# Kernel tuning notes

Measured on AMD Instinct MI355X. Metric: run time of the kernel, lower is better.

Reference implementation:

```python
import jax, jax.numpy as jnp
import numpy as np

B, T, C = 16, 64, 512


def setup_inputs() -> dict:
    key = jax.random.key(0)
    ks = jax.random.split(key, 12)
    s = 1.0 / np.sqrt(C)
    st = 1.0 / np.sqrt(2.0)
    return {
        "x": jax.random.normal(ks[0], (B, T, C), dtype=jnp.float32),
        "ts": jax.random.uniform(ks[1], (B, T), dtype=jnp.float32),
        "attn_mask": jnp.ones((B, T), dtype=jnp.float32),
        # project: Linear(C, C)
        "W_proj": jax.random.uniform(ks[2], (C, C), jnp.float32, -s, s),
        "b_proj": jax.random.uniform(ks[3], (C,), jnp.float32, -s, s),
        # embed_xs: Linear(C, C)
        "W_x": jax.random.uniform(ks[4], (C, C), jnp.float32, -s, s),
        "b_x": jax.random.uniform(ks[5], (C,), jnp.float32, -s, s),
        # embed_ts: Linear(2, C)
        "W_t": jax.random.uniform(ks[6], (2, C), jnp.float32, -st, st),
        "b_t": jax.random.uniform(ks[7], (C,), jnp.float32, -st, st),
        # get_importances Linear(C, C)
        "W_imp": jax.random.uniform(ks[8], (C, C), jnp.float32, -s, s),
        "b_imp": jax.random.uniform(ks[9], (C,), jnp.float32, -s, s),
    }


def reference(x, ts, attn_mask, W_proj, b_proj, W_x, b_x, W_t, b_t, W_imp, b_imp):
    # x: [B,T,C], ts: [B,T], attn_mask: [B,T]
    values = (x @ W_proj + b_proj)[:, None, :, :]          # [B,1,T,C]
    rel = ts[:, :, None] - ts[:, None, :]                  # [B,T,T]
    rel2 = jnp.log1p(jnp.maximum(jnp.stack([rel, -rel], axis=-1), 0.0))  # [B,T,T,2]
    h = rel2 @ W_t + b_t                                   # [B,T,T,C] (include_t)
    h = h + (x @ W_x + b_x)[:, None, :, :]                 # include_x, broadcast over dim 1
    importances = jax.nn.sigmoid(jax.nn.relu(h) @ W_imp + b_imp)  # [B,T,T,C]
    importances = importances * attn_mask[:, None, :, None]
    interactions = jax.nn.logsumexp(values * importances, axis=2)  # [B,T,C]
    return (x + interactions, importances.mean(axis=3))
```

## Files before the change

### kernel.cpp

```cpp
#include <hip/hip_runtime.h>
#include <hip/hip_bf16.h>

#define Bn 16
#define Tn 64
#define Cn 512
#define LDA  520
#define LDA8 528

#define LOG2E 1.4426950408889634f
#define LN2   0.6931471805599453f
#define ASC 16.0f
#define WSC 256.0f
#define ZSC (1.0f/4096.0f)
#define NZL (-(LOG2E)*(ZSC))
#define SC1 0x7F7F7F7FU

typedef short s8v __attribute__((ext_vector_type(8)));
typedef float f4v __attribute__((ext_vector_type(4)));
typedef int   i8v __attribute__((ext_vector_type(8)));

__device__ __forceinline__ unsigned int pk2bf(float a, float b){
  __hip_bfloat162 t = __float22bfloat162_rn(make_float2(a, b));
  union { __hip_bfloat162 h; unsigned int u; } c; c.h = t; return c.u;
}
__device__ __forceinline__ float bits2f(unsigned int u){
  union { unsigned int u; float f; } c; c.u = u; return c.f;
}
__device__ __forceinline__ s8v pack_bf8(const float* v){
  union { uint4 u; s8v s; } c;
  c.u.x = pk2bf(v[0], v[1]); c.u.y = pk2bf(v[2], v[3]);
  c.u.z = pk2bf(v[4], v[5]); c.u.w = pk2bf(v[6], v[7]);
  return c.s;
}
union U8 { uint4 q[2]; i8v v; };

__global__ __launch_bounds__(512)
void pre(const float* __restrict__ x, const float* __restrict__ ts,
         const float* __restrict__ Wp, const float* __restrict__ bp,
         const float* __restrict__ Wx, const float* __restrict__ bx,
         const float* __restrict__ bt, const float* __restrict__ Wi,
         float* __restrict__ xe, unsigned short* __restrict__ vfrag,
         unsigned char* __restrict__ Wsw8, float* __restrict__ R){
  __shared__ unsigned short lA[Tn * LDA];
  const int blk = blockIdx.x;
  const int tid = threadIdx.x;
  if(blk < 32){
    int gid2 = blk * 512 + tid;
    float r[8];
#pragma unroll
    for(int q = 0; q < 4; ++q){
      int p = gid2 * 4 + q;
      int b = p >> 12, i = (p >> 6) & 63, j = p & 63;
      float d = ts[b * Tn + i] - ts[b * Tn + j];
      r[2*q]   = __logf(1.f + fmaxf(d, 0.f));
      r[2*q+1] = __logf(1.f + fmaxf(-d, 0.f));
    }
    float4* Rf4 = reinterpret_cast<float4*>(R);
    Rf4[gid2 * 2    ] = make_float4(r[0], r[1], r[2], r[3]);
    Rf4[gid2 * 2 + 1] = make_float4(r[4], r[5], r[6], r[7]);
    return;
  }
  if(blk < 64){
    int rem = (blk - 32) * 512 + tid;
    int p    = rem & 1;
    int lane = (rem >> 1) & 63;
    int t    = (rem >> 7) & 31;
    int s128 = rem >> 12;
    int quad = lane >> 4, ln = lane & 15;
    int k0 = s128 * 128 + quad * 32 + p * 16;
    int n  = t * 16 + ln;
    float v[16];
#pragma unroll
    for(int j = 0; j < 16; ++j) v[j] = Wi[(k0 + j) * Cn + n] * WSC;
    unsigned int d[4];
#pragma unroll
    for(int g = 0; g < 4; ++g){
      int dd = __builtin_amdgcn_cvt_pk_fp8_f32(v[4*g],   v[4*g+1], 0, false);
      dd     = __builtin_amdgcn_cvt_pk_fp8_f32(v[4*g+2], v[4*g+3], dd, true);
      d[g] = (unsigned int)dd;
    }
    uint4 o; o.x = d[0]; o.y = d[1]; o.z = d[2]; o.w = d[3];
    *reinterpret_cast<uint4*>(Wsw8 + (size_t)(s128 * 32 + t) * 2048 + p * 1024 + lane * 16) = o;
    return;
  }
  const int idx = blk - 64;
  const int b = idx >> 3, mat = (idx >> 2) & 1, half = idx & 3;
  const int lane = tid & 63, w = tid >> 6, quad = lane >> 4, ln = lane & 15;
  const int t = half * 8 + w;
  const float* Wg = mat ? Wx : Wp;
  const float* wb = Wg + (size_t)(quad * 8) * Cn + t * 16 + ln;

  const int c0 = (tid & 127) * 4, jb = tid >> 7;
#pragma unroll
  for(int it = 0; it < 16; ++it){
    int j = jb + it * 4;
    f4v xv = *reinterpret_cast<const f4v*>(x + ((b * Tn + j) * Cn + c0));
    uint2 uu; uu.x = pk2bf(xv[0], xv[1]); uu.y = pk2bf(xv[2], xv[3]);
    *reinterpret_cast<uint2*>(&lA[j * LDA + c0]) = uu;
  }
  float wv[8];
#pragma unroll
  for(int j = 0; j < 8; ++j) wv[j] = wb[j * Cn];
  __syncthreads();

  s8v a[4], an[4];
#pragma unroll
  for(int mt = 0; mt < 4; ++mt)
    a[mt] = *reinterpret_cast<const s8v*>(&lA[(mt * 16 + ln) * LDA + quad * 8]);
  f4v acc[4];
#pragma unroll
  for(int mt = 0; mt < 4; ++mt){ acc[mt][0]=0.f; acc[mt][1]=0.f; acc[mt][2]=0.f; acc[mt][3]=0.f; }
  s8v bcur = pack_bf8(wv);

#pragma unroll 2
  for(int s = 0; s < 16; ++s){
    int sn = (s + 1) & 15;
    float wn[8];
#pragma unroll
    for(int j = 0; j < 8; ++j) wn[j] = wb[(size_t)sn * 32 * Cn + j * Cn];
#pragma unroll
    for(int mt = 0; mt < 4; ++mt)
      an[mt] = *reinterpret_cast<const s8v*>(&lA[(mt * 16 + ln) * LDA + sn * 32 + quad * 8]);
#pragma unroll
    for(int mt = 0; mt < 4; ++mt)
      acc[mt] = __builtin_amdgcn_mfma_f32_16x16x32_bf16(a[mt], bcur, acc[mt], 0, 0, 0);
#pragma unroll
    for(int mt = 0; mt < 4; ++mt) a[mt] = an[mt];
    bcur = pack_bf8(wn);
  }

  const int c = t * 16 + ln;
  const int oct = t >> 2, w2 = t & 3;
  if(mat == 0){
    float bb = bp[c];
    const int eb_h = w2 & 1;
#pragma unroll
    for(int mt = 0; mt < 4; ++mt){
      float v0 = (acc[mt][0] + bb) * LOG2E;
      float v1 = (acc[mt][1] + bb) * LOG2E;
      float v2 = (acc[mt][2] + bb) * LOG2E;
      float v3 = (acc[mt][3] + bb) * LOG2E;
      uint2 o; o.x = pk2bf(v0, v1); o.y = pk2bf(v2, v3);
      int eb = mt * 2 + (w2 >> 1);
      *reinterpret_cast<uint2*>(vfrag + ((size_t)((b * 8 + oct) * 8 + eb) * 64 + lane) * 8 + eb_h * 4) = o;
    }
  } else {
    float bb = bx[c] + bt[c];
#pragma unroll
    for(int mt = 0; mt < 4; ++mt)
#pragma unroll
      for(int r = 0; r < 4; ++r){
        int j = mt * 16 + quad * 4 + r;
        xe[(b * Tn + j) * Cn + c] = (acc[mt][r] + bb) * ASC;
      }
  }
}

__global__ __launch_bounds__(512, 4)
void fused(const float* __restrict__ x, const float* __restrict__ am,
           const float* __restrict__ Wt, const float* __restrict__ bimp,
           const unsigned char* __restrict__ Wsw8, const float* __restrict__ R,
           const float* __restrict__ xe, const unsigned short* __restrict__ vfrag,
           float* __restrict__ out0, float* __restrict__ out1){
  __shared__ unsigned char lA8[Tn * LDA8];
  __shared__ float msk[Tn], rr0[Tn], rr1[Tn], rsum[Tn];
  const int b = blockIdx.x >> 6, i = blockIdx.x & 63;
  const int tid = threadIdx.x;
  const int lane = tid & 63, w = tid >> 6, quad = lane >> 4, ln = lane & 15;
  const int st = blockIdx.x & 3;

  float mv = 0.f; float2 rv = make_float2(0.f, 0.f);
  if(tid < Tn){
    mv = am[b * Tn + tid];
    rv = reinterpret_cast<const float2*>(R)[(b * Tn + i) * Tn + tid];
  }

  const int c0 = (tid & 127) * 4, jb = tid >> 7;
  f4v xv[16];
#pragma unroll
  for(int it = 0; it < 16; ++it)
    xv[it] = *reinterpret_cast<const f4v*>(xe + ((b * Tn + (jb + it * 4)) * Cn + c0));

  if(tid < Tn){ msk[tid] = mv; rr0[tid] = rv.x; rr1[tid] = rv.y; rsum[tid] = 0.f; }
  __syncthreads();

  f4v wt0 = *reinterpret_cast<const f4v*>(Wt + c0);
  f4v wt1 = *reinterpret_cast<const f4v*>(Wt + Cn + c0);
  wt0[0]*=ASC; wt0[1]*=ASC; wt0[2]*=ASC; wt0[3]*=ASC;
  wt1[0]*=ASC; wt1[1]*=ASC; wt1[2]*=ASC; wt1[3]*=ASC;
#pragma unroll
  for(int it = 0; it < 16; ++it){
    int j = jb + it * 4;
    float r0 = rr0[j], r1 = rr1[j];
    float h0 = fmaxf(fmaf(r1, wt1[0], fmaf(r0, wt0[0], xv[it][0])), 0.f);
    float h1 = fmaxf(fmaf(r1, wt1[1], fmaf(r0, wt0[1], xv[it][1])), 0.f);
    float h2 = fmaxf(fmaf(r1, wt1[2], fmaf(r0, wt0[2], xv[it][2])), 0.f);
    float h3 = fmaxf(fmaf(r1, wt1[3], fmaf(r0, wt0[3], xv[it][3])), 0.f);
    int d = __builtin_amdgcn_cvt_pk_fp8_f32(h0, h1, 0, false);
    d     = __builtin_amdgcn_cvt_pk_fp8_f32(h2, h3, d, true);
    *reinterpret_cast<int*>(lA8 + j * LDA8 + c0) = d;
  }
  __syncthreads();

  f4v acc[4][4];
#pragma unroll
  for(int mt = 0; mt < 4; ++mt)
#pragma unroll
    for(int nt = 0; nt < 4; ++nt){
      acc[mt][nt][0]=0.f; acc[mt][nt][1]=0.f; acc[mt][nt][2]=0.f; acc[mt][nt][3]=0.f;
    }

#pragma unroll 1
  for(int sI = 0; sI < 4; ++sI){
    const int s128 = (st + sI) & 3;
    U8 ub0, ub1, ub2, ub3;
    const unsigned char* Bb = Wsw8 + (size_t)(s128 * 32 + w * 4) * 2048 + lane * 16;
    ub0.q[0] = *reinterpret_cast<const uint4*>(Bb);
    ub0.q[1] = *reinterpret_cast<const uint4*>(Bb + 1024);
    ub1.q[0] = *reinterpret_cast<const uint4*>(Bb + 2048);
    ub1.q[1] = *reinterpret_cast<const uint4*>(Bb + 3072);
    ub2.q[0] = *reinterpret_cast<const uint4*>(Bb + 4096);
    ub2.q[1] = *reinterpret_cast<const uint4*>(Bb + 5120);
    ub3.q[0] = *reinterpret_cast<const uint4*>(Bb + 6144);
    ub3.q[1] = *reinterpret_cast<const uint4*>(Bb + 7168);
#pragma unroll
    for(int mt = 0; mt < 4; ++mt){
      U8 ua;
      const unsigned char* ap = lA8 + (mt * 16 + ln) * LDA8 + s128 * 128 + quad * 32;
      ua.q[0] = *reinterpret_cast<const uint4*>(ap);
      ua.q[1] = *reinterpret_cast<const uint4*>(ap + 16);
      acc[mt][0] = __builtin_amdgcn_mfma_scale_f32_16x16x128_f8f6f4(ua.v, ub0.v, acc[mt][0], 0, 0, 0, SC1, 0, SC1);
      acc[mt][1] = __builtin_amdgcn_mfma_scale_f32_16x16x128_f8f6f4(ua.v, ub1.v, acc[mt][1], 0, 0, 0, SC1, 0, SC1);
      acc[mt][2] = __builtin_amdgcn_mfma_scale_f32_16x16x128_f8f6f4(ua.v, ub2.v, acc[mt][2], 0, 0, 0, SC1, 0, SC1);
      acc[mt][3] = __builtin_amdgcn_mfma_scale_f32_16x16x128_f8f6f4(ua.v, ub3.v, acc[mt][3], 0, 0, 0, SC1, 0, SC1);
    }
  }

  uint4 vv[8];
#pragma unroll
  for(int eb = 0; eb < 8; ++eb)
    vv[eb] = *reinterpret_cast<const uint4*>(vfrag + ((size_t)((b * 8 + w) * 8 + eb) * 64 + lane) * 8);
  float xq[4];
#pragma unroll
  for(int nt = 0; nt < 4; ++nt)
    xq[nt] = x[(b * Tn + i) * Cn + (w * 64 + nt * 16 + ln)];

  const unsigned int* vw = reinterpret_cast<const unsigned int*>(vv);
  float bbf[4];
#pragma unroll
  for(int nt = 0; nt < 4; ++nt) bbf[nt] = bimp[w * 64 + nt * 16 + ln] * -LOG2E;
  float se[4] = {0.f, 0.f, 0.f, 0.f};
#pragma unroll
  for(int mt = 0; mt < 4; ++mt)
#pragma unroll
    for(int r = 0; r < 4; ++r){
      float mk = msk[mt * 16 + quad * 4 + r];
      float p = 0.f;
#pragma unroll
      for(int nt = 0; nt < 4; ++nt){
        float zn = fmaf(acc[mt][nt][r], NZL, bbf[nt]);
        float im = mk * __builtin_amdgcn_rcpf(1.f + __builtin_amdgcn_exp2f(zn));
        p += im;
        int e = mt * 16 + nt * 4 + r;
        unsigned int d = vw[e >> 1];
        float vl = bits2f((e & 1) ? (d & 0xffff0000u) : (d << 16));
        se[nt] += __builtin_amdgcn_exp2f(vl * im);
      }
      p += __shfl_xor(p, 1, 64);
      p += __shfl_xor(p, 2, 64);
      p += __shfl_xor(p, 4, 64);
      p += __shfl_xor(p, 8, 64);
      if(ln == 0) atomicAdd(&rsum[mt * 16 + quad * 4 + r], p);
    }
  __syncthreads();
  if(tid < Tn) out1[(b * Tn + i) * Tn + tid] = rsum[tid] * (1.f / 512.f);

#pragma unroll
  for(int nt = 0; nt < 4; ++nt){
    float s0 = se[nt];
    s0 += __shfl_xor(s0, 16, 64);
    s0 += __shfl_xor(s0, 32, 64);
    if(quad == 0){
      int idx = (b * Tn + i) * Cn + (w * 64 + nt * 16 + ln);
      out0[idx] = xq[nt] + __builtin_amdgcn_logf(s0) * LN2;
    }
  }
}

extern "C" void kernel_launch(void* const* d_in, const int* in_sizes, int n_in,
                              void* d_out, int out_size, void* d_ws, size_t ws_size,
                              hipStream_t stream){
  const float* x    = (const float*)d_in[0];
  const float* ts   = (const float*)d_in[1];
  const float* am   = (const float*)d_in[2];
  const float* Wp   = (const float*)d_in[3];
  const float* bp   = (const float*)d_in[4];
  const float* Wx   = (const float*)d_in[5];
  const float* bx   = (const float*)d_in[6];
  const float* Wt   = (const float*)d_in[7];
  const float* bt   = (const float*)d_in[8];
  const float* Wi   = (const float*)d_in[9];
  const float* bimp = (const float*)d_in[10];
  float* out0 = (float*)d_out;
  float* out1 = out0 + Bn * Tn * Cn;

  char* ws = (char*)d_ws;
  unsigned char*  Wsw8  = (unsigned char*)ws;
  float*          xe    = (float*)(ws + 262144);
  unsigned short* vfrag = (unsigned short*)(ws + 2359296);
  float*          R     = (float*)(ws + 3407872);

  pre<<<192, 512, 0, stream>>>(x, ts, Wp, bp, Wx, bx, bt, Wi, xe, vfrag, Wsw8, R);
  fused<<<1024, 512, 0, stream>>>(x, am, Wt, bimp, Wsw8, R, xe, vfrag, out0, out1);
}
```

Baseline: 118.9 us.

## Use 1024-thread blocks with 16 waves each owning 32 output columns and prefetch B

Doubles the block size of the fused kernel to 16 waves, so each wave computes a 64x32 tile instead of 64x64. This halves per-thread accumulators, B fragments and epilogue work. It also software-prefetches the next K-slice of the fp8 weight fragments into registers while the current MFMAs run. The goal is more latency hiding and lower register pressure per wave. The cost is heavier block-level synchronisation, and launch_bounds(1024,4) may force register spilling or cap occupancy.

```diff
diff --git a/kernel.cpp b/kernel.cpp
--- a/kernel.cpp
+++ b/kernel.cpp
@@ -156,7 +156,7 @@
   }
 }
 
-__global__ __launch_bounds__(512, 4)
+__global__ __launch_bounds__(1024, 4)
 void fused(const float* __restrict__ x, const float* __restrict__ am,
            const float* __restrict__ Wt, const float* __restrict__ bimp,
            const unsigned char* __restrict__ Wsw8, const float* __restrict__ R,
@@ -168,18 +168,28 @@
   const int tid = threadIdx.x;
   const int lane = tid & 63, w = tid >> 6, quad = lane >> 4, ln = lane & 15;
   const int st = blockIdx.x & 3;
+  const int bi = b * Tn + i;
 
   float mv = 0.f; float2 rv = make_float2(0.f, 0.f);
   if(tid < Tn){
     mv = am[b * Tn + tid];
-    rv = reinterpret_cast<const float2*>(R)[(b * Tn + i) * Tn + tid];
+    rv = reinterpret_cast<const float2*>(R)[(size_t)bi * Tn + tid];
+  }
+
+  U8 cb0, cb1;
+  {
+    const unsigned char* Bb = Wsw8 + (size_t)(st * 32 + w * 2) * 2048 + (size_t)lane * 16;
+    cb0.q[0] = *reinterpret_cast<const uint4*>(Bb);
+    cb0.q[1] = *reinterpret_cast<const uint4*>(Bb + 1024);
+    cb1.q[0] = *reinterpret_cast<const uint4*>(Bb + 2048);
+    cb1.q[1] = *reinterpret_cast<const uint4*>(Bb + 3072);
   }
 
   const int c0 = (tid & 127) * 4, jb = tid >> 7;
-  f4v xv[16];
-#pragma unroll
-  for(int it = 0; it < 16; ++it)
-    xv[it] = *reinterpret_cast<const f4v*>(xe + ((b * Tn + (jb + it * 4)) * Cn + c0));
+  f4v xv[8];
+#pragma unroll
+  for(int it = 0; it < 8; ++it)
+    xv[it] = *reinterpret_cast<const f4v*>(xe + ((size_t)(b * Tn + (jb + it * 8)) * Cn + c0));
 
   if(tid < Tn){ msk[tid] = mv; rr0[tid] = rv.x; rr1[tid] = rv.y; rsum[tid] = 0.f; }
   __syncthreads();
@@ -189,8 +199,8 @@
   wt0[0]*=ASC; wt0[1]*=ASC; wt0[2]*=ASC; wt0[3]*=ASC;
   wt1[0]*=ASC; wt1[1]*=ASC; wt1[2]*=ASC; wt1[3]*=ASC;
 #pragma unroll
-  for(int it = 0; it < 16; ++it){
-    int j = jb + it * 4;
+  for(int it = 0; it < 8; ++it){
+    int j = jb + it * 8;
     float r0 = rr0[j], r1 = rr1[j];
     float h0 = fmaxf(fmaf(r1, wt1[0], fmaf(r0, wt0[0], xv[it][0])), 0.f);
     float h1 = fmaxf(fmaf(r1, wt1[1], fmaf(r0, wt0[1], xv[it][1])), 0.f);
@@ -202,54 +212,53 @@
   }
   __syncthreads();
 
-  f4v acc[4][4];
+  f4v acc[4][2];
 #pragma unroll
   for(int mt = 0; mt < 4; ++mt)
 #pragma unroll
-    for(int nt = 0; nt < 4; ++nt){
+    for(int nt = 0; nt < 2; ++nt){
       acc[mt][nt][0]=0.f; acc[mt][nt][1]=0.f; acc[mt][nt][2]=0.f; acc[mt][nt][3]=0.f;
     }
 
 #pragma unroll 1
   for(int sI = 0; sI < 4; ++sI){
     const int s128 = (st + sI) & 3;
-    U8 ub0, ub1, ub2, ub3;
-    const unsigned char* Bb = Wsw8 + (size_t)(s128 * 32 + w * 4) * 2048 + lane * 16;
-    ub0.q[0] = *reinterpret_cast<const uint4*>(Bb);
-    ub0.q[1] = *reinterpret_cast<const uint4*>(Bb + 1024);
-    ub1.q[0] = *reinterpret_cast<const uint4*>(Bb + 2048);
-    ub1.q[1] = *reinterpret_cast<const uint4*>(Bb + 3072);
-    ub2.q[0] = *reinterpret_cast<const uint4*>(Bb + 4096);
-    ub2.q[1] = *reinterpret_cast<const uint4*>(Bb + 5120);
-    ub3.q[0] = *reinterpret_cast<const uint4*>(Bb + 6144);
-    ub3.q[1] = *reinterpret_cast<const uint4*>(Bb + 7168);
+    U8 nb0, nb1;
+    if(sI < 3){
+      const int sn = (st + sI + 1) & 3;
+      const unsigned char* Bn2 = Wsw8 + (size_t)(sn * 32 + w * 2) * 2048 + (size_t)lane * 16;
+      nb0.q[0] = *reinterpret_cast<const uint4*>(Bn2);
+      nb0.q[1] = *reinterpret_cast<const uint4*>(Bn2 + 1024);
+      nb1.q[0] = *reinterpret_cast<const uint4*>(Bn2 + 2048);
+      nb1.q[1] = *reinterpret_cast<const uint4*>(Bn2 + 3072);
+    }
 #pragma unroll
     for(int mt = 0; mt < 4; ++mt){
       U8 ua;
       const unsigned char* ap = lA8 + (mt * 16 + ln) * LDA8 + s128 * 128 + quad * 32;
       ua.q[0] = *reinterpret_cast<const uint4*>(ap);
       ua.q[1] = *reinterpret_cast<const uint4*>(ap + 16);
-      acc[mt][0] = __builtin_amdgcn_mfma_scale_f32_16x16x128_f8f6f4(ua.v, ub0.v, acc[mt][0], 0, 0, 0, SC1, 0, SC1);
-      acc[mt][1] = __builtin_amdgcn_mfma_scale_f32_16x16x128_f8f6f4(ua.v, ub1.v, acc[mt][1], 0, 0, 0, SC1, 0, SC1);
-      acc[mt][2] = __builtin_amdgcn_mfma_scale_f32_16x16x128_f8f6f4(ua.v, ub2.v, acc[mt][2], 0, 0, 0, SC1, 0, SC1);
-      acc[mt][3] = __builtin_amdgcn_mfma_scale_f32_16x16x128_f8f6f4(ua.v, ub3.v, acc[mt][3], 0, 0, 0, SC1, 0, SC1);
-    }
-  }
-
-  uint4 vv[8];
-#pragma unroll
-  for(int eb = 0; eb < 8; ++eb)
-    vv[eb] = *reinterpret_cast<const uint4*>(vfrag + ((size_t)((b * 8 + w) * 8 + eb) * 64 + lane) * 8);
-  float xq[4];
-#pragma unroll
-  for(int nt = 0; nt < 4; ++nt)
-    xq[nt] = x[(b * Tn + i) * Cn + (w * 64 + nt * 16 + ln)];
+      acc[mt][0] = __builtin_amdgcn_mfma_scale_f32_16x16x128_f8f6f4(ua.v, cb0.v, acc[mt][0], 0, 0, 0, SC1, 0, SC1);
+      acc[mt][1] = __builtin_amdgcn_mfma_scale_f32_16x16x128_f8f6f4(ua.v, cb1.v, acc[mt][1], 0, 0, 0, SC1, 0, SC1);
+    }
+    if(sI < 3){ cb0 = nb0; cb1 = nb1; }
+  }
+
+  uint4 vv[4];
+#pragma unroll
+  for(int mt = 0; mt < 4; ++mt)
+    vv[mt] = *reinterpret_cast<const uint4*>(
+        vfrag + ((size_t)((b * 8 + (w >> 1)) * 8 + (mt * 2 + (w & 1))) * 64 + lane) * 8);
+  float xq[2];
+#pragma unroll
+  for(int nt = 0; nt < 2; ++nt)
+    xq[nt] = x[(size_t)bi * Cn + (w * 32 + nt * 16 + ln)];
 
   const unsigned int* vw = reinterpret_cast<const unsigned int*>(vv);
-  float bbf[4];
-#pragma unroll
-  for(int nt = 0; nt < 4; ++nt) bbf[nt] = bimp[w * 64 + nt * 16 + ln] * -LOG2E;
-  float se[4] = {0.f, 0.f, 0.f, 0.f};
+  float bbf[2];
+#pragma unroll
+  for(int nt = 0; nt < 2; ++nt) bbf[nt] = bimp[w * 32 + nt * 16 + ln] * -LOG2E;
+  float se[2] = {0.f, 0.f};
 #pragma unroll
   for(int mt = 0; mt < 4; ++mt)
 #pragma unroll
@@ -257,13 +266,12 @@
       float mk = msk[mt * 16 + quad * 4 + r];
       float p = 0.f;
 #pragma unroll
-      for(int nt = 0; nt < 4; ++nt){
+      for(int nt = 0; nt < 2; ++nt){
         float zn = fmaf(acc[mt][nt][r], NZL, bbf[nt]);
         float im = mk * __builtin_amdgcn_rcpf(1.f + __builtin_amdgcn_exp2f(zn));
         p += im;
-        int e = mt * 16 + nt * 4 + r;
-        unsigned int d = vw[e >> 1];
-        float vl = bits2f((e & 1) ? (d & 0xffff0000u) : (d << 16));
+        unsigned int d = vw[mt * 4 + nt * 2 + (r >> 1)];
+        float vl = bits2f((r & 1) ? (d & 0xffff0000u) : (d << 16));
         se[nt] += __builtin_amdgcn_exp2f(vl * im);
       }
       p += __shfl_xor(p, 1, 64);
@@ -273,15 +281,15 @@
       if(ln == 0) atomicAdd(&rsum[mt * 16 + quad * 4 + r], p);
     }
   __syncthreads();
-  if(tid < Tn) out1[(b * Tn + i) * Tn + tid] = rsum[tid] * (1.f / 512.f);
-
-#pragma unroll
-  for(int nt = 0; nt < 4; ++nt){
+  if(tid < Tn) out1[(size_t)bi * Tn + tid] = rsum[tid] * (1.f / 512.f);
+
+#pragma unroll
+  for(int nt = 0; nt < 2; ++nt){
     float s0 = se[nt];
     s0 += __shfl_xor(s0, 16, 64);
     s0 += __shfl_xor(s0, 32, 64);
     if(quad == 0){
-      int idx = (b * Tn + i) * Cn + (w * 64 + nt * 16 + ln);
+      int idx = bi * Cn + (w * 32 + nt * 16 + ln);
       out0[idx] = xq[nt] + __builtin_amdgcn_logf(s0) * LN2;
     }
   }
@@ -311,5 +319,5 @@
   float*          R     = (float*)(ws + 3407872);
 
   pre<<<192, 512, 0, stream>>>(x, ts, Wp, bp, Wx, bx, bt, Wi, xe, vfrag, Wsw8, R);
-  fused<<<1024, 512, 0, stream>>>(x, am, Wt, bimp, Wsw8, R, xe, vfrag, out0, out1);
-}
+  fused<<<1024, 1024, 0, stream>>>(x, am, Wt, bimp, Wsw8, R, xe, vfrag, out0, out1);
+}
```

Result: slower. 130.1 us (+9.3%).
